# Optimization experiments

Hardware: AMD Instinct MI355X
Metric: run time of the kernel (lower is better)

## Reference

```python
import jax, jax.numpy as jnp
import numpy as np

N = 50000
E = 800000
IN_FEATS = 256
NUM_HEADS = 4
OUT_FEATS = 64
NUM_ETYPES = 8
ALPHA = 100.0
NEG_SLOPE_ATTN = 0.2   # self.leaky_relu
NEG_SLOPE_EW = 0.01    # nn.LeakyReLU() default, applied to edge weights


def leaky_relu(x, slope):
    return jnp.where(x >= 0, x, slope * x)


def setup_inputs() -> dict:
    key = jax.random.key(0)
    ks = jax.random.split(key, 8)
    feat = jax.random.normal(ks[0], (N, IN_FEATS), dtype=jnp.float32)
    src = jax.random.randint(ks[1], (E,), 0, N, dtype=jnp.int32)
    dst = jax.random.randint(ks[2], (E,), 0, N, dtype=jnp.int32)
    # etypes are 1-indexed in the original code (edge_weight[edge_feats - 1])
    edge_feats = jax.random.randint(ks[3], (E,), 1, NUM_ETYPES + 1, dtype=jnp.int32)
    # parameters (xavier-normal-ish init for weights; edge_weight = 1/alpha)
    fc_w = jax.random.normal(ks[4], (NUM_HEADS * OUT_FEATS, IN_FEATS), dtype=jnp.float32) * 0.05
    attn_l = jax.random.normal(ks[5], (1, NUM_HEADS, OUT_FEATS), dtype=jnp.float32) * 0.1
    attn_r = jax.random.normal(ks[6], (1, NUM_HEADS, OUT_FEATS), dtype=jnp.float32) * 0.1
    edge_weight = jnp.full((NUM_ETYPES, NUM_HEADS), 1.0 / ALPHA, dtype=jnp.float32)
    return {"feat": feat, "src": src, "dst": dst, "edge_feats": edge_feats,
            "fc_w": fc_w, "attn_l": attn_l, "attn_r": attn_r, "edge_weight": edge_weight}


def reference(feat, src, dst, edge_feats, fc_w, attn_l, attn_r, edge_weight):
    # feat: [N, F_in] -> ft: [N, H, D]
    ft = (feat @ fc_w.T).reshape(-1, NUM_HEADS, OUT_FEATS)
    el = jnp.einsum('nhd,ohd->nh', ft, attn_l)  # [N, H]
    er = jnp.einsum('nhd,ohd->nh', ft, attn_r)  # [N, H]
    # edge-type weights (1-indexed), scaled & leaky-relu'd
    ew = leaky_relu(edge_weight * ALPHA, NEG_SLOPE_EW)  # [T, H]
    ee = ew[edge_feats - 1]                              # [E, H]
    # per-edge logits: u_add_v, times edge weight, leaky relu
    e = leaky_relu((el[src] + er[dst]) * ee, NEG_SLOPE_ATTN)  # [E, H]
    # edge softmax grouped by destination node
    emax = jax.ops.segment_max(e, dst, num_segments=N)        # [N, H]
    ex = jnp.exp(e - emax[dst])
    denom = jax.ops.segment_sum(ex, dst, num_segments=N)      # [N, H]
    a = ex / denom[dst]                                        # [E, H]
    # weighted scatter-sum: sum over edges of a * ft[src]
    msg = ft[src] * a[:, :, None]                              # [E, H, D]
    rst = jax.ops.segment_sum(msg, dst, num_segments=N)       # [N, H, D]
    return rst
```

## Files before the change

### kernel.cpp

```cpp
#include <hip/hip_runtime.h>
#include <hip/hip_bf16.h>


#define NF 256
#define HD 256
#define NH 4
#define PB 256

typedef __attribute__((ext_vector_type(8))) short short8;
typedef __attribute__((ext_vector_type(4))) float f32x4;

static __device__ __forceinline__ unsigned short f2bf(float f) {
  unsigned int u = __float_as_uint(f);
  u += 0x7FFFu + ((u >> 16) & 1u);
  return (unsigned short)(u >> 16);
}
static __device__ __forceinline__ float bf2f(unsigned short s) {
  return __uint_as_float(((unsigned int)s) << 16);
}
static __device__ __forceinline__ unsigned pkbf(float a, float b) {
  __hip_bfloat162 h = __float22bfloat162_rn(make_float2(a, b));
  return *(unsigned*)&h;
}
static __device__ __forceinline__ float wcalc(float sum, float ew) {
  float x = sum * ew;
  x = (x >= 0.f) ? x : 0.2f * x;
  return __expf(x);
}

__global__ __launch_bounds__(256) void part_hist_k(
    const int* __restrict__ dst, const float* __restrict__ w,
    unsigned short* __restrict__ o, int* __restrict__ ghist, int e, int epb) {
  __shared__ int bins[256];
  int tid = threadIdx.x, blk = blockIdx.x;
  bins[tid] = 0;
  int ci = blk * 256 + tid;
  if (ci < 16384) {
    float4 v = ((const float4*)w)[ci];
    ((uint2*)o)[ci] = make_uint2(pkbf(v.x, v.y), pkbf(v.z, v.w));
  }
  __syncthreads();
  int e0 = blk * epb, e1 = e0 + epb; if (e1 > e) e1 = e;
  for (int i = e0 + tid; i < e1; i += 256)
    atomicAdd(&bins[dst[i] >> 8], 1);
  __syncthreads();
  ghist[tid * PB + blk] = bins[tid];
}

__global__ __launch_bounds__(1024) void scan2_k(const int* __restrict__ in,
                                                int* __restrict__ outp, int n) {
  __shared__ int wtot[16];
  __shared__ int wexcl[16];
  __shared__ int ctot;
  int tid = threadIdx.x, lane = tid & 63, wid = tid >> 6;
  int carry = 0;
  int nchunk = (n + 8191) >> 13;
  for (int c = 0; c < nchunk; ++c) {
    int base = (c << 13) + tid * 8;
    int v[8];
    if (base + 8 <= n) {
      int4 a = *(const int4*)(in + base);
      int4 b = *(const int4*)(in + base + 4);
      v[0] = a.x; v[1] = a.y; v[2] = a.z; v[3] = a.w;
      v[4] = b.x; v[5] = b.y; v[6] = b.z; v[7] = b.w;
    } else {
#pragma unroll
      for (int j = 0; j < 8; ++j) v[j] = (base + j < n) ? in[base + j] : 0;
    }
    int p[8]; int run = 0;
#pragma unroll
    for (int j = 0; j < 8; ++j) { run += v[j]; p[j] = run; }
    int incl = run;
#pragma unroll
    for (int off = 1; off < 64; off <<= 1) {
      int t = __shfl_up(incl, off);
      if (lane >= off) incl += t;
    }
    if (lane == 63) wtot[wid] = incl;
    __syncthreads();
    if (wid == 0 && lane < 16) {
      int wv = wtot[lane]; int wi = wv;
#pragma unroll
      for (int off = 1; off < 16; off <<= 1) {
        int t = __shfl_up(wi, off);
        if (lane >= off) wi += t;
      }
      wexcl[lane] = wi - wv;
      if (lane == 15) ctot = wi;
    }
    __syncthreads();
    int ebase = carry + wexcl[wid] + (incl - run);
#pragma unroll
    for (int j = 0; j < 8; ++j) {
      int i = base + j;
      if (i < n) outp[i] = ebase + p[j] - v[j];
    }
    carry += ctot;
    __syncthreads();
  }
  if (tid == 0) outp[n] = carry;
}

__global__ __launch_bounds__(256) void part_scatter_k(
    const int* __restrict__ src, const int* __restrict__ dst,
    const int* __restrict__ efeats, const int* __restrict__ sg,
    int* __restrict__ mid, int e, int epb) {
  __shared__ int cur[256];
  int tid = threadIdx.x, blk = blockIdx.x;
  cur[tid] = sg[tid * PB + blk];
  __syncthreads();
  int e0 = blk * epb, e1 = e0 + epb; if (e1 > e) e1 = e;
  for (int i = e0 + tid; i < e1; i += 256) {
    int d = dst[i];
    int pos = atomicAdd(&cur[d >> 8], 1);
    mid[pos] = src[i] | ((efeats[i] - 1) << 17) | ((d & 255) << 20);
  }
}

__global__ __launch_bounds__(256) void bucket_k(
    const int* __restrict__ mid, const int* __restrict__ sg,
    int* __restrict__ poffs, int* __restrict__ pk, int nN) {
  __shared__ int cnt[256];
  __shared__ int cur[256];
  int tid = threadIdx.x, b = blockIdx.x;
  int bb0 = sg[b * PB];
  int bb1 = sg[(b + 1) * PB];
  cnt[tid] = 0;
  __syncthreads();
  for (int i = bb0 + tid; i < bb1; i += 256)
    atomicAdd(&cnt[(mid[i] >> 20) & 255], 1);
  __syncthreads();
  if (tid < 64) {
    int carry = 0;
#pragma unroll
    for (int c = 0; c < 4; ++c) {
      int v = cnt[c * 64 + tid];
      int inc = v;
#pragma unroll
      for (int off = 1; off < 64; off <<= 1) {
        int t2 = __shfl_up(inc, off);
        if (tid >= off) inc += t2;
      }
      cur[c * 64 + tid] = inc - v + carry;
      carry += __shfl(inc, 63);
    }
  }
  __syncthreads();
  int node = b * 256 + tid;
  int g = bb0 + cur[tid];
  if (node <= nN) poffs[node] = g;
  cur[tid] = g;
  __syncthreads();
  for (int i = bb0 + tid; i < bb1; i += 256) {
    int v = mid[i];
    int pos = atomicAdd(&cur[(v >> 20) & 255], 1);
    pk[pos] = v & 0xFFFFF;
  }
}

__global__ __launch_bounds__(256) void gemm_k(
    const float* __restrict__ feat, const unsigned short* __restrict__ fcb,
    const float* __restrict__ attn_l, const float* __restrict__ attn_r,
    unsigned short* __restrict__ ftb, float* __restrict__ el,
    float* __restrict__ er, int n) {
  __shared__ short aF[4 * 2 * 64 * 8];
  __shared__ short bF[16 * 2 * 64 * 8];
  int tid = threadIdx.x;
  int lane = tid & 63, w = tid >> 6;
  int row0 = blockIdx.x * 64;

  f32x4 acc[4][4];
#pragma unroll
  for (int i = 0; i < 4; ++i)
#pragma unroll
    for (int j = 0; j < 4; ++j) acc[i][j] = (f32x4){0.f, 0.f, 0.f, 0.f};

  int ar = tid >> 2, ak = (tid & 3) << 4;
  int arow = row0 + ar; if (arow >= n) arow = n - 1;
  const float* ap = feat + (size_t)arow * NF + ak;
  int am = ar & 15, art = ar >> 4;
  int s0 = ak >> 5, q0 = (ak >> 3) & 3;
  int s1 = (ak + 8) >> 5, q1 = ((ak + 8) >> 3) & 3;
  short* aw0 = &aF[(((art * 2 + s0) * 64) + q0 * 16 + am) * 8];
  short* aw1 = &aF[(((art * 2 + s1) * 64) + q1 * 16 + am) * 8];

  const unsigned short* bp = fcb + (size_t)tid * NF;
  int bn = tid & 15, bcg = tid >> 4;

  for (int k0 = 0; k0 < NF; k0 += 64) {
    float4 f0 = *(const float4*)(ap + k0);
    float4 f1 = *(const float4*)(ap + k0 + 4);
    float4 f2 = *(const float4*)(ap + k0 + 8);
    float4 f3 = *(const float4*)(ap + k0 + 12);
    uint4 oa = make_uint4(pkbf(f0.x, f0.y), pkbf(f0.z, f0.w),
                          pkbf(f1.x, f1.y), pkbf(f1.z, f1.w));
    uint4 ob = make_uint4(pkbf(f2.x, f2.y), pkbf(f2.z, f2.w),
                          pkbf(f3.x, f3.y), pkbf(f3.z, f3.w));
    *(uint4*)aw0 = oa;
    *(uint4*)aw1 = ob;
#pragma unroll
    for (int o8 = 0; o8 < 8; ++o8) {
      short8 bv = *(const short8*)(bp + k0 + o8 * 8);
      int bs = o8 >> 2, bq = o8 & 3;
      *(short8*)&bF[(((bcg * 2 + bs) * 64) + bq * 16 + bn) * 8] = bv;
    }
    __syncthreads();
#pragma unroll
    for (int s = 0; s < 2; ++s) {
      short8 af[4], bfr[4];
#pragma unroll
      for (int rt = 0; rt < 4; ++rt)
        af[rt] = *(const short8*)&aF[(((rt * 2 + s) * 64) + lane) * 8];
#pragma unroll
      for (int ct = 0; ct < 4; ++ct)
        bfr[ct] = *(const short8*)&bF[((((w * 4 + ct) * 2 + s) * 64) + lane) * 8];
#pragma unroll
      for (int rt = 0; rt < 4; ++rt)
#pragma unroll
        for (int ct = 0; ct < 4; ++ct)
          acc[rt][ct] = __builtin_amdgcn_mfma_f32_16x16x32_bf16(
              af[rt], bfr[ct], acc[rt][ct], 0, 0, 0);
    }
    __syncthreads();
  }

  int ln = lane & 15, lq = lane >> 4;
  float al4[4], ar4[4];
#pragma unroll
  for (int ct = 0; ct < 4; ++ct) {
    al4[ct] = attn_l[w * 64 + ct * 16 + ln];
    ar4[ct] = attn_r[w * 64 + ct * 16 + ln];
  }
#pragma unroll
  for (int rt = 0; rt < 4; ++rt) {
#pragma unroll
    for (int r = 0; r < 4; ++r) {
      float pl = 0.f, pr = 0.f;
#pragma unroll
      for (int ct = 0; ct < 4; ++ct) {
        float v = acc[rt][ct][r];
        pl += v * al4[ct]; pr += v * ar4[ct];
      }
#pragma unroll
      for (int off = 1; off <= 8; off <<= 1) {
        pl += __shfl_xor(pl, off);
        pr += __shfl_xor(pr, off);
      }
      int row = row0 + rt * 16 + lq * 4 + r;
      if (row < n) {
        if (ln == 0) { el[row * NH + w] = pl; er[row * NH + w] = pr; }
        unsigned short* fr = ftb + (size_t)row * HD + w * 64 + ln;
#pragma unroll
        for (int ct = 0; ct < 4; ++ct) fr[ct * 16] = f2bf(acc[rt][ct][r]);
      }
    }
  }
}

__global__ __launch_bounds__(256) void agg3_k(
    const unsigned short* __restrict__ ftb, const int* __restrict__ pk,
    const float* __restrict__ el, const float* __restrict__ er,
    const float* __restrict__ ewt, const int* __restrict__ offs,
    float* __restrict__ out, int n) {
  __shared__ float ew_s[32];
  if (threadIdx.x < 32) {
    float v = ewt[threadIdx.x] * 100.0f;
    ew_s[threadIdx.x] = (v >= 0.f) ? v : 0.01f * v;
  }
  __syncthreads();
  int node = blockIdx.x * 4 + (threadIdx.x >> 6);
  int lane = threadIdx.x & 63;
  if (node >= n) return;
  int start = offs[node];
  int deg = offs[node + 1] - start;
  float o0 = 0.f, o1 = 0.f, o2 = 0.f, o3 = 0.f;
  if (deg > 0) {
    int hl = lane >> 4;
    float er_h = er[(size_t)node * NH + hl];
    const unsigned short* fb = ftb + (size_t)lane * 4;
    const float* elh = el + hl;
    const int* pg = pk + start;
    float ss = 0.f;
    int i = 0;
    for (; i + 8 <= deg; i += 8) {
      int4 pa = *(const int4*)(pg + i);
      int4 pb = *(const int4*)(pg + i + 4);
      int sA = pa.x & 0x1FFFF, tA = pa.x >> 17;
      int sB = pa.y & 0x1FFFF, tB = pa.y >> 17;
      int sC = pa.z & 0x1FFFF, tC = pa.z >> 17;
      int sD = pa.w & 0x1FFFF, tD = pa.w >> 17;
      int sE = pb.x & 0x1FFFF, tE = pb.x >> 17;
      int sF = pb.y & 0x1FFFF, tF = pb.y >> 17;
      int sG = pb.z & 0x1FFFF, tG = pb.z >> 17;
      int sH = pb.w & 0x1FFFF, tH = pb.w >> 17;
      float eA = elh[sA * NH], eB = elh[sB * NH], eC = elh[sC * NH], eD = elh[sD * NH];
      float eE = elh[sE * NH], eF = elh[sF * NH], eG = elh[sG * NH], eH = elh[sH * NH];
      ushort4 fA = *(const ushort4*)(fb + (size_t)sA * HD);
      ushort4 fB = *(const ushort4*)(fb + (size_t)sB * HD);
      ushort4 fC = *(const ushort4*)(fb + (size_t)sC * HD);
      ushort4 fD = *(const ushort4*)(fb + (size_t)sD * HD);
      ushort4 fE = *(const ushort4*)(fb + (size_t)sE * HD);
      ushort4 fF = *(const ushort4*)(fb + (size_t)sF * HD);
      ushort4 fG = *(const ushort4*)(fb + (size_t)sG * HD);
      ushort4 fH = *(const ushort4*)(fb + (size_t)sH * HD);
      float wA = wcalc(eA + er_h, ew_s[tA * NH + hl]);
      float wB = wcalc(eB + er_h, ew_s[tB * NH + hl]);
      float wC = wcalc(eC + er_h, ew_s[tC * NH + hl]);
      float wD = wcalc(eD + er_h, ew_s[tD * NH + hl]);
      float wE = wcalc(eE + er_h, ew_s[tE * NH + hl]);
      float wF = wcalc(eF + er_h, ew_s[tF * NH + hl]);
      float wG = wcalc(eG + er_h, ew_s[tG * NH + hl]);
      float wH = wcalc(eH + er_h, ew_s[tH * NH + hl]);
      ss += ((wA + wB) + (wC + wD)) + ((wE + wF) + (wG + wH));
      o0 = fmaf(wA, bf2f(fA.x), o0); o1 = fmaf(wA, bf2f(fA.y), o1);
      o2 = fmaf(wA, bf2f(fA.z), o2); o3 = fmaf(wA, bf2f(fA.w), o3);
      o0 = fmaf(wB, bf2f(fB.x), o0); o1 = fmaf(wB, bf2f(fB.y), o1);
      o2 = fmaf(wB, bf2f(fB.z), o2); o3 = fmaf(wB, bf2f(fB.w), o3);
      o0 = fmaf(wC, bf2f(fC.x), o0); o1 = fmaf(wC, bf2f(fC.y), o1);
      o2 = fmaf(wC, bf2f(fC.z), o2); o3 = fmaf(wC, bf2f(fC.w), o3);
      o0 = fmaf(wD, bf2f(fD.x), o0); o1 = fmaf(wD, bf2f(fD.y), o1);
      o2 = fmaf(wD, bf2f(fD.z), o2); o3 = fmaf(wD, bf2f(fD.w), o3);
      o0 = fmaf(wE, bf2f(fE.x), o0); o1 = fmaf(wE, bf2f(fE.y), o1);
      o2 = fmaf(wE, bf2f(fE.z), o2); o3 = fmaf(wE, bf2f(fE.w), o3);
      o0 = fmaf(wF, bf2f(fF.x), o0); o1 = fmaf(wF, bf2f(fF.y), o1);
      o2 = fmaf(wF, bf2f(fF.z), o2); o3 = fmaf(wF, bf2f(fF.w), o3);
      o0 = fmaf(wG, bf2f(fG.x), o0); o1 = fmaf(wG, bf2f(fG.y), o1);
      o2 = fmaf(wG, bf2f(fG.z), o2); o3 = fmaf(wG, bf2f(fG.w), o3);
      o0 = fmaf(wH, bf2f(fH.x), o0); o1 = fmaf(wH, bf2f(fH.y), o1);
      o2 = fmaf(wH, bf2f(fH.z), o2); o3 = fmaf(wH, bf2f(fH.w), o3);
    }
    for (; i < deg; ++i) {
      int pv = pg[i];
      int sA = pv & 0x1FFFF, tA = pv >> 17;
      float eA = elh[sA * NH];
      ushort4 fA = *(const ushort4*)(fb + (size_t)sA * HD);
      float wA = wcalc(eA + er_h, ew_s[tA * NH + hl]);
      ss += wA;
      o0 = fmaf(wA, bf2f(fA.x), o0); o1 = fmaf(wA, bf2f(fA.y), o1);
      o2 = fmaf(wA, bf2f(fA.z), o2); o3 = fmaf(wA, bf2f(fA.w), o3);
    }
    float rs = 1.0f / ss;
    o0 *= rs; o1 *= rs; o2 *= rs; o3 *= rs;
  }
  *(float4*)(out + (size_t)node * HD + lane * 4) = make_float4(o0, o1, o2, o3);
}

extern "C" void kernel_launch(void* const* d_in, const int* in_sizes, int n_in,
                              void* d_out, int out_size, void* d_ws, size_t ws_size,
                              hipStream_t stream) {
  const float* feat   = (const float*)d_in[0];
  const int*   src    = (const int*)d_in[1];
  const int*   dst    = (const int*)d_in[2];
  const int*   efeats = (const int*)d_in[3];
  const float* fc_w   = (const float*)d_in[4];
  const float* attn_l = (const float*)d_in[5];
  const float* attn_r = (const float*)d_in[6];
  const float* ewt    = (const float*)d_in[7];
  float* out = (float*)d_out;

  int N = in_sizes[0] / NF;
  int E = in_sizes[1];

  char* ws = (char*)d_ws;
  size_t off = 0;
  unsigned short* fcb = (unsigned short*)(ws + off); off += (size_t)NF * HD * 2;
  unsigned short* ftb = (unsigned short*)(ws + off); off += (size_t)N * HD * 2;
  float* el  = (float*)(ws + off);  off += (size_t)N * NH * 4;
  float* er  = (float*)(ws + off);  off += (size_t)N * NH * 4;
  int* poffs = (int*)(ws + off);    off += ((size_t)N + 16) * 4;
  int* ghist = (int*)(ws + off);    off += (size_t)PB * 256 * 4;
  int* sg    = (int*)(ws + off);    off += ((size_t)PB * 256 + 8) * 4;
  int* mid   = (int*)(ws + off);    off += (size_t)E * 4;
  int* pk    = (int*)(ws + off);    off += (size_t)E * 4;

  int epb = (E + PB - 1) / PB;
  int NB = (N >> 8) + 1;

  part_hist_k<<<PB, 256, 0, stream>>>(dst, fc_w, fcb, ghist, E, epb);
  scan2_k<<<1, 1024, 0, stream>>>(ghist, sg, PB * 256);
  part_scatter_k<<<PB, 256, 0, stream>>>(src, dst, efeats, sg, mid, E, epb);
  bucket_k<<<NB, 256, 0, stream>>>(mid, sg, poffs, pk, N);
  gemm_k<<<(N + 63) / 64, 256, 0, stream>>>(feat, fcb, attn_l, attn_r, ftb, el, er, N);
  agg3_k<<<(N + 3) / 4, 256, 0, stream>>>(ftb, pk, el, er, ewt, poffs, out, N);
}
```

Baseline: 270.7 us.

## Fuse all stages into one persistent cooperative kernel with grid syncs

Merges the six separate launches (histogram, scan, partition scatter, bucket sort, GEMM, aggregation) into one cooperative persistent kernel. Stages are separated by grid-wide barriers, and work is spread with grid-stride loops. The single-block global scan becomes a two-level multi-block scan. This aims to remove per-launch gaps and the serial scan bottleneck. In exchange it pays for grid-barrier latency, an occupancy query on every call, and a register cap from the launch bounds that may slow the GEMM and aggregation phases. The old multi-kernel path is kept as a fallback.

```diff
diff --git a/kernel.cpp b/kernel.cpp
--- a/kernel.cpp
+++ b/kernel.cpp
@@ -1,11 +1,13 @@
 #include <hip/hip_runtime.h>
 #include <hip/hip_bf16.h>
+#include <hip/hip_cooperative_groups.h>
+
+namespace cg = cooperative_groups;
 
 
 #define NF 256
 #define HD 256
 #define NH 4
-#define PB 256
 
 typedef __attribute__((ext_vector_type(8))) short short8;
 typedef __attribute__((ext_vector_type(4))) float f32x4;
@@ -28,147 +30,12 @@
   return __expf(x);
 }
 
-__global__ __launch_bounds__(256) void part_hist_k(
-    const int* __restrict__ dst, const float* __restrict__ w,
-    unsigned short* __restrict__ o, int* __restrict__ ghist, int e, int epb) {
-  __shared__ int bins[256];
-  int tid = threadIdx.x, blk = blockIdx.x;
-  bins[tid] = 0;
-  int ci = blk * 256 + tid;
-  if (ci < 16384) {
-    float4 v = ((const float4*)w)[ci];
-    ((uint2*)o)[ci] = make_uint2(pkbf(v.x, v.y), pkbf(v.z, v.w));
-  }
-  __syncthreads();
-  int e0 = blk * epb, e1 = e0 + epb; if (e1 > e) e1 = e;
-  for (int i = e0 + tid; i < e1; i += 256)
-    atomicAdd(&bins[dst[i] >> 8], 1);
-  __syncthreads();
-  ghist[tid * PB + blk] = bins[tid];
-}
-
-__global__ __launch_bounds__(1024) void scan2_k(const int* __restrict__ in,
-                                                int* __restrict__ outp, int n) {
-  __shared__ int wtot[16];
-  __shared__ int wexcl[16];
-  __shared__ int ctot;
-  int tid = threadIdx.x, lane = tid & 63, wid = tid >> 6;
-  int carry = 0;
-  int nchunk = (n + 8191) >> 13;
-  for (int c = 0; c < nchunk; ++c) {
-    int base = (c << 13) + tid * 8;
-    int v[8];
-    if (base + 8 <= n) {
-      int4 a = *(const int4*)(in + base);
-      int4 b = *(const int4*)(in + base + 4);
-      v[0] = a.x; v[1] = a.y; v[2] = a.z; v[3] = a.w;
-      v[4] = b.x; v[5] = b.y; v[6] = b.z; v[7] = b.w;
-    } else {
-#pragma unroll
-      for (int j = 0; j < 8; ++j) v[j] = (base + j < n) ? in[base + j] : 0;
-    }
-    int p[8]; int run = 0;
-#pragma unroll
-    for (int j = 0; j < 8; ++j) { run += v[j]; p[j] = run; }
-    int incl = run;
-#pragma unroll
-    for (int off = 1; off < 64; off <<= 1) {
-      int t = __shfl_up(incl, off);
-      if (lane >= off) incl += t;
-    }
-    if (lane == 63) wtot[wid] = incl;
-    __syncthreads();
-    if (wid == 0 && lane < 16) {
-      int wv = wtot[lane]; int wi = wv;
-#pragma unroll
-      for (int off = 1; off < 16; off <<= 1) {
-        int t = __shfl_up(wi, off);
-        if (lane >= off) wi += t;
-      }
-      wexcl[lane] = wi - wv;
-      if (lane == 15) ctot = wi;
-    }
-    __syncthreads();
-    int ebase = carry + wexcl[wid] + (incl - run);
-#pragma unroll
-    for (int j = 0; j < 8; ++j) {
-      int i = base + j;
-      if (i < n) outp[i] = ebase + p[j] - v[j];
-    }
-    carry += ctot;
-    __syncthreads();
-  }
-  if (tid == 0) outp[n] = carry;
-}
-
-__global__ __launch_bounds__(256) void part_scatter_k(
-    const int* __restrict__ src, const int* __restrict__ dst,
-    const int* __restrict__ efeats, const int* __restrict__ sg,
-    int* __restrict__ mid, int e, int epb) {
-  __shared__ int cur[256];
-  int tid = threadIdx.x, blk = blockIdx.x;
-  cur[tid] = sg[tid * PB + blk];
-  __syncthreads();
-  int e0 = blk * epb, e1 = e0 + epb; if (e1 > e) e1 = e;
-  for (int i = e0 + tid; i < e1; i += 256) {
-    int d = dst[i];
-    int pos = atomicAdd(&cur[d >> 8], 1);
-    mid[pos] = src[i] | ((efeats[i] - 1) << 17) | ((d & 255) << 20);
-  }
-}
-
-__global__ __launch_bounds__(256) void bucket_k(
-    const int* __restrict__ mid, const int* __restrict__ sg,
-    int* __restrict__ poffs, int* __restrict__ pk, int nN) {
-  __shared__ int cnt[256];
-  __shared__ int cur[256];
-  int tid = threadIdx.x, b = blockIdx.x;
-  int bb0 = sg[b * PB];
-  int bb1 = sg[(b + 1) * PB];
-  cnt[tid] = 0;
-  __syncthreads();
-  for (int i = bb0 + tid; i < bb1; i += 256)
-    atomicAdd(&cnt[(mid[i] >> 20) & 255], 1);
-  __syncthreads();
-  if (tid < 64) {
-    int carry = 0;
-#pragma unroll
-    for (int c = 0; c < 4; ++c) {
-      int v = cnt[c * 64 + tid];
-      int inc = v;
-#pragma unroll
-      for (int off = 1; off < 64; off <<= 1) {
-        int t2 = __shfl_up(inc, off);
-        if (tid >= off) inc += t2;
-      }
-      cur[c * 64 + tid] = inc - v + carry;
-      carry += __shfl(inc, 63);
-    }
-  }
-  __syncthreads();
-  int node = b * 256 + tid;
-  int g = bb0 + cur[tid];
-  if (node <= nN) poffs[node] = g;
-  cur[tid] = g;
-  __syncthreads();
-  for (int i = bb0 + tid; i < bb1; i += 256) {
-    int v = mid[i];
-    int pos = atomicAdd(&cur[(v >> 20) & 255], 1);
-    pk[pos] = v & 0xFFFFF;
-  }
-}
-
-__global__ __launch_bounds__(256) void gemm_k(
-    const float* __restrict__ feat, const unsigned short* __restrict__ fcb,
-    const float* __restrict__ attn_l, const float* __restrict__ attn_r,
-    unsigned short* __restrict__ ftb, float* __restrict__ el,
-    float* __restrict__ er, int n) {
-  __shared__ short aF[4 * 2 * 64 * 8];
-  __shared__ short bF[16 * 2 * 64 * 8];
-  int tid = threadIdx.x;
+
+static __device__ __forceinline__ void gemm_tile(
+    const float* feat, const unsigned short* fcb, const float* attn_l,
+    const float* attn_r, unsigned short* ftb, float* el, float* er,
+    int n, int row0, int tid, short* aF, short* bF) {
   int lane = tid & 63, w = tid >> 6;
-  int row0 = blockIdx.x * 64;
-
   f32x4 acc[4][4];
 #pragma unroll
   for (int i = 0; i < 4; ++i)
@@ -257,22 +124,11 @@
   }
 }
 
-__global__ __launch_bounds__(256) void agg3_k(
-    const unsigned short* __restrict__ ftb, const int* __restrict__ pk,
-    const float* __restrict__ el, const float* __restrict__ er,
-    const float* __restrict__ ewt, const int* __restrict__ offs,
-    float* __restrict__ out, int n) {
-  __shared__ float ew_s[32];
-  if (threadIdx.x < 32) {
-    float v = ewt[threadIdx.x] * 100.0f;
-    ew_s[threadIdx.x] = (v >= 0.f) ? v : 0.01f * v;
-  }
-  __syncthreads();
-  int node = blockIdx.x * 4 + (threadIdx.x >> 6);
-  int lane = threadIdx.x & 63;
-  if (node >= n) return;
-  int start = offs[node];
-  int deg = offs[node + 1] - start;
+static __device__ __forceinline__ void agg_node(
+    const unsigned short* ftb, const int* pk, const float* el, const float* er,
+    const float* ew_s, const int* poffs, float* out, int node, int lane) {
+  int start = poffs[node];
+  int deg = poffs[node + 1] - start;
   float o0 = 0.f, o1 = 0.f, o2 = 0.f, o3 = 0.f;
   if (deg > 0) {
     int hl = lane >> 4;
@@ -345,6 +201,327 @@
   *(float4*)(out + (size_t)node * HD + lane * 4) = make_float4(o0, o1, o2, o3);
 }
 
+
+__global__ __launch_bounds__(256, 4) void mega_k(
+    const float* __restrict__ feat, const float* __restrict__ fc_w,
+    const int* __restrict__ src, const int* __restrict__ dst,
+    const int* __restrict__ efeats, const float* __restrict__ attn_l,
+    const float* __restrict__ attn_r, const float* __restrict__ ewt,
+    unsigned short* fcb, unsigned short* ftb, float* el, float* er,
+    int* ghist, int* sg, int* btot, int* bbase, int* mid, int* pk,
+    int* poffs, float* out, int n, int e) {
+  cg::grid_group gg = cg::this_grid();
+  __shared__ __align__(16) char smem[40960];
+  int tid = threadIdx.x, blk = blockIdx.x;
+  int nblk = gridDim.x;
+  int lane = tid & 63, wid = tid >> 6;
+  int epb = (e + nblk - 1) / nblk;
+  int e0 = blk * epb, e1 = e0 + epb; if (e1 > e) e1 = e;
+
+  {
+    int* bins = (int*)smem;
+    bins[tid] = 0;
+    int ci = blk * 256 + tid;
+    if (ci < 16384) {
+      float4 v = ((const float4*)fc_w)[ci];
+      ((uint2*)fcb)[ci] = make_uint2(pkbf(v.x, v.y), pkbf(v.z, v.w));
+    }
+    __syncthreads();
+    for (int i = e0 + tid; i < e1; i += 256)
+      atomicAdd(&bins[dst[i] >> 8], 1);
+    __syncthreads();
+    ghist[tid * nblk + blk] = bins[tid];
+  }
+  gg.sync();
+
+  {
+    int* wt = (int*)smem;
+    int v = ghist[blk * 256 + tid];
+    int inc = v;
+#pragma unroll
+    for (int off = 1; off < 64; off <<= 1) {
+      int t = __shfl_up(inc, off);
+      if (lane >= off) inc += t;
+    }
+    if (lane == 63) wt[wid] = inc;
+    __syncthreads();
+    int base = 0;
+    if (wid > 0) base += wt[0];
+    if (wid > 1) base += wt[1];
+    if (wid > 2) base += wt[2];
+    sg[blk * 256 + tid] = base + inc - v;
+    if (tid == 255) btot[blk] = base + inc;
+  }
+  gg.sync();
+
+  if (blk == 0) {
+    int* wt = (int*)smem;
+    int per = nblk >> 8;
+    int vals[4]; int run = 0;
+#pragma unroll
+    for (int k = 0; k < 4; ++k) {
+      vals[k] = (k < per) ? btot[tid * per + k] : 0;
+      run += vals[k];
+    }
+    int inc = run;
+#pragma unroll
+    for (int off = 1; off < 64; off <<= 1) {
+      int t = __shfl_up(inc, off);
+      if (lane >= off) inc += t;
+    }
+    if (lane == 63) wt[wid] = inc;
+    __syncthreads();
+    int base = 0;
+    if (wid > 0) base += wt[0];
+    if (wid > 1) base += wt[1];
+    if (wid > 2) base += wt[2];
+    int eb = base + inc - run;
+#pragma unroll
+    for (int k = 0; k < 4; ++k)
+      if (k < per) { bbase[tid * per + k] = eb; eb += vals[k]; }
+  }
+  gg.sync();
+
+  {
+    int* cur = (int*)smem;
+    int j = tid * nblk + blk;
+    cur[tid] = sg[j] + bbase[j >> 8];
+    __syncthreads();
+    for (int i = e0 + tid; i < e1; i += 256) {
+      int d = dst[i];
+      int pos = atomicAdd(&cur[d >> 8], 1);
+      mid[pos] = src[i] | ((efeats[i] - 1) << 17) | ((d & 255) << 20);
+    }
+  }
+  gg.sync();
+
+  {
+    int nbuck = (n + 255) >> 8;
+    int* cnt = (int*)smem;
+    int* cur = (int*)smem + 256;
+    for (int b = blk; b < nbuck; b += nblk) {
+      int j0 = b * nblk, j1 = (b + 1) * nblk;
+      int bb0 = sg[j0] + bbase[j0 >> 8];
+      int bb1 = sg[j1] + bbase[j1 >> 8];
+      cnt[tid] = 0;
+      __syncthreads();
+      for (int i = bb0 + tid; i < bb1; i += 256)
+        atomicAdd(&cnt[(mid[i] >> 20) & 255], 1);
+      __syncthreads();
+      if (tid < 64) {
+        int carry = 0;
+#pragma unroll
+        for (int c = 0; c < 4; ++c) {
+          int v = cnt[c * 64 + tid];
+          int inc = v;
+#pragma unroll
+          for (int off = 1; off < 64; off <<= 1) {
+            int t2 = __shfl_up(inc, off);
+            if (tid >= off) inc += t2;
+          }
+          cur[c * 64 + tid] = inc - v + carry;
+          carry += __shfl(inc, 63);
+        }
+      }
+      __syncthreads();
+      int node = b * 256 + tid;
+      int gv = bb0 + cur[tid];
+      if (node <= n) poffs[node] = gv;
+      cur[tid] = gv;
+      __syncthreads();
+      for (int i = bb0 + tid; i < bb1; i += 256) {
+        int v = mid[i];
+        int pos = atomicAdd(&cur[(v >> 20) & 255], 1);
+        pk[pos] = v & 0xFFFFF;
+      }
+      __syncthreads();
+    }
+  }
+  __syncthreads();
+
+  {
+    short* aF = (short*)smem;
+    short* bF = (short*)(smem + 8192);
+    for (int t = blk; t * 64 < n; t += nblk)
+      gemm_tile(feat, fcb, attn_l, attn_r, ftb, el, er, n, t * 64, tid, aF, bF);
+  }
+  gg.sync();
+
+  {
+    float* ew_s = (float*)smem;
+    if (tid < 32) {
+      float v = ewt[tid] * 100.0f;
+      ew_s[tid] = (v >= 0.f) ? v : 0.01f * v;
+    }
+    __syncthreads();
+    for (int nb = blk * 4; nb < n; nb += nblk * 4) {
+      int node = nb + wid;
+      if (node < n) agg_node(ftb, pk, el, er, ew_s, poffs, out, node, lane);
+    }
+  }
+}
+
+
+__global__ __launch_bounds__(256) void part_hist_k(
+    const int* __restrict__ dst, const float* __restrict__ w,
+    unsigned short* __restrict__ o, int* __restrict__ ghist, int e, int epb,
+    int pb) {
+  __shared__ int bins[256];
+  int tid = threadIdx.x, blk = blockIdx.x;
+  bins[tid] = 0;
+  int ci = blk * 256 + tid;
+  if (ci < 16384) {
+    float4 v = ((const float4*)w)[ci];
+    ((uint2*)o)[ci] = make_uint2(pkbf(v.x, v.y), pkbf(v.z, v.w));
+  }
+  __syncthreads();
+  int e0 = blk * epb, e1 = e0 + epb; if (e1 > e) e1 = e;
+  for (int i = e0 + tid; i < e1; i += 256)
+    atomicAdd(&bins[dst[i] >> 8], 1);
+  __syncthreads();
+  ghist[tid * pb + blk] = bins[tid];
+}
+
+__global__ __launch_bounds__(1024) void scan2_k(const int* __restrict__ in,
+                                                int* __restrict__ outp, int n) {
+  __shared__ int wtot[16];
+  __shared__ int wexcl[16];
+  __shared__ int ctot;
+  int tid = threadIdx.x, lane = tid & 63, wid = tid >> 6;
+  int carry = 0;
+  int nchunk = (n + 8191) >> 13;
+  for (int c = 0; c < nchunk; ++c) {
+    int base = (c << 13) + tid * 8;
+    int v[8];
+    if (base + 8 <= n) {
+      int4 a = *(const int4*)(in + base);
+      int4 b = *(const int4*)(in + base + 4);
+      v[0] = a.x; v[1] = a.y; v[2] = a.z; v[3] = a.w;
+      v[4] = b.x; v[5] = b.y; v[6] = b.z; v[7] = b.w;
+    } else {
+#pragma unroll
+      for (int j = 0; j < 8; ++j) v[j] = (base + j < n) ? in[base + j] : 0;
+    }
+    int p[8]; int run = 0;
+#pragma unroll
+    for (int j = 0; j < 8; ++j) { run += v[j]; p[j] = run; }
+    int incl = run;
+#pragma unroll
+    for (int off = 1; off < 64; off <<= 1) {
+      int t = __shfl_up(incl, off);
+      if (lane >= off) incl += t;
+    }
+    if (lane == 63) wtot[wid] = incl;
+    __syncthreads();
+    if (wid == 0 && lane < 16) {
+      int wv = wtot[lane]; int wi = wv;
+#pragma unroll
+      for (int off = 1; off < 16; off <<= 1) {
+        int t = __shfl_up(wi, off);
+        if (lane >= off) wi += t;
+      }
+      wexcl[lane] = wi - wv;
+      if (lane == 15) ctot = wi;
+    }
+    __syncthreads();
+    int ebase = carry + wexcl[wid] + (incl - run);
+#pragma unroll
+    for (int j = 0; j < 8; ++j) {
+      int i = base + j;
+      if (i < n) outp[i] = ebase + p[j] - v[j];
+    }
+    carry += ctot;
+    __syncthreads();
+  }
+  if (tid == 0) outp[n] = carry;
+}
+
+__global__ __launch_bounds__(256) void part_scatter_k(
+    const int* __restrict__ src, const int* __restrict__ dst,
+    const int* __restrict__ efeats, const int* __restrict__ sg,
+    int* __restrict__ mid, int e, int epb, int pb) {
+  __shared__ int cur[256];
+  int tid = threadIdx.x, blk = blockIdx.x;
+  cur[tid] = sg[tid * pb + blk];
+  __syncthreads();
+  int e0 = blk * epb, e1 = e0 + epb; if (e1 > e) e1 = e;
+  for (int i = e0 + tid; i < e1; i += 256) {
+    int d = dst[i];
+    int pos = atomicAdd(&cur[d >> 8], 1);
+    mid[pos] = src[i] | ((efeats[i] - 1) << 17) | ((d & 255) << 20);
+  }
+}
+
+__global__ __launch_bounds__(256) void bucket_k(
+    const int* __restrict__ mid, const int* __restrict__ sg,
+    int* __restrict__ poffs, int* __restrict__ pk, int nN, int pb) {
+  __shared__ int cnt[256];
+  __shared__ int cur[256];
+  int tid = threadIdx.x, b = blockIdx.x;
+  int bb0 = sg[b * pb];
+  int bb1 = sg[(b + 1) * pb];
+  cnt[tid] = 0;
+  __syncthreads();
+  for (int i = bb0 + tid; i < bb1; i += 256)
+    atomicAdd(&cnt[(mid[i] >> 20) & 255], 1);
+  __syncthreads();
+  if (tid < 64) {
+    int carry = 0;
+#pragma unroll
+    for (int c = 0; c < 4; ++c) {
+      int v = cnt[c * 64 + tid];
+      int inc = v;
+#pragma unroll
+      for (int off = 1; off < 64; off <<= 1) {
+        int t2 = __shfl_up(inc, off);
+        if (tid >= off) inc += t2;
+      }
+      cur[c * 64 + tid] = inc - v + carry;
+      carry += __shfl(inc, 63);
+    }
+  }
+  __syncthreads();
+  int node = b * 256 + tid;
+  int g = bb0 + cur[tid];
+  if (node <= nN) poffs[node] = g;
+  cur[tid] = g;
+  __syncthreads();
+  for (int i = bb0 + tid; i < bb1; i += 256) {
+    int v = mid[i];
+    int pos = atomicAdd(&cur[(v >> 20) & 255], 1);
+    pk[pos] = v & 0xFFFFF;
+  }
+}
+
+__global__ __launch_bounds__(256) void gemm_k(
+    const float* __restrict__ feat, const unsigned short* __restrict__ fcb,
+    const float* __restrict__ attn_l, const float* __restrict__ attn_r,
+    unsigned short* __restrict__ ftb, float* __restrict__ el,
+    float* __restrict__ er, int n) {
+  __shared__ short aF[4 * 2 * 64 * 8];
+  __shared__ short bF[16 * 2 * 64 * 8];
+  gemm_tile(feat, fcb, attn_l, attn_r, ftb, el, er, n,
+            blockIdx.x * 64, threadIdx.x, aF, bF);
+}
+
+__global__ __launch_bounds__(256) void agg3_k(
+    const unsigned short* __restrict__ ftb, const int* __restrict__ pk,
+    const float* __restrict__ el, const float* __restrict__ er,
+    const float* __restrict__ ewt, const int* __restrict__ offs,
+    float* __restrict__ out, int n) {
+  __shared__ float ew_s[32];
+  if (threadIdx.x < 32) {
+    float v = ewt[threadIdx.x] * 100.0f;
+    ew_s[threadIdx.x] = (v >= 0.f) ? v : 0.01f * v;
+  }
+  __syncthreads();
+  int node = blockIdx.x * 4 + (threadIdx.x >> 6);
+  int lane = threadIdx.x & 63;
+  if (node >= n) return;
+  agg_node(ftb, pk, el, er, ew_s, offs, out, node, lane);
+}
+
+
 extern "C" void kernel_launch(void* const* d_in, const int* in_sizes, int n_in,
                               void* d_out, int out_size, void* d_ws, size_t ws_size,
                               hipStream_t stream) {
@@ -368,18 +545,36 @@
   float* el  = (float*)(ws + off);  off += (size_t)N * NH * 4;
   float* er  = (float*)(ws + off);  off += (size_t)N * NH * 4;
   int* poffs = (int*)(ws + off);    off += ((size_t)N + 16) * 4;
-  int* ghist = (int*)(ws + off);    off += (size_t)PB * 256 * 4;
-  int* sg    = (int*)(ws + off);    off += ((size_t)PB * 256 + 8) * 4;
+  int* ghist = (int*)(ws + off);    off += (size_t)1024 * 256 * 4;
+  int* sg    = (int*)(ws + off);    off += ((size_t)1024 * 256 + 8) * 4;
+  int* btot  = (int*)(ws + off);    off += 1024 * 4;
+  int* bbase = (int*)(ws + off);    off += 1024 * 4;
   int* mid   = (int*)(ws + off);    off += (size_t)E * 4;
   int* pk    = (int*)(ws + off);    off += (size_t)E * 4;
 
-  int epb = (E + PB - 1) / PB;
-  int NB = (N >> 8) + 1;
-
-  part_hist_k<<<PB, 256, 0, stream>>>(dst, fc_w, fcb, ghist, E, epb);
-  scan2_k<<<1, 1024, 0, stream>>>(ghist, sg, PB * 256);
-  part_scatter_k<<<PB, 256, 0, stream>>>(src, dst, efeats, sg, mid, E, epb);
-  bucket_k<<<NB, 256, 0, stream>>>(mid, sg, poffs, pk, N);
-  gemm_k<<<(N + 63) / 64, 256, 0, stream>>>(feat, fcb, attn_l, attn_r, ftb, el, er, N);
-  agg3_k<<<(N + 3) / 4, 256, 0, stream>>>(ftb, pk, el, er, ewt, poffs, out, N);
-}
+  int occ = 0;
+  hipError_t oerr = hipOccupancyMaxActiveBlocksPerMultiprocessor(&occ, mega_k, 256, 0);
+  bool coop_ok = (oerr == hipSuccess) && (occ >= 1);
+  if (coop_ok) {
+    if (occ > 4) occ = 4;
+    int nblk = occ * 256;
+    void* args[] = {&feat, &fc_w, &src, &dst, &efeats, &attn_l, &attn_r, &ewt,
+                    &fcb, &ftb, &el, &er, &ghist, &sg, &btot, &bbase,
+                    &mid, &pk, &poffs, &out, &N, &E};
+    hipError_t lerr = hipLaunchCooperativeKernel(mega_k, dim3(nblk), dim3(256),
+                                                 args, 0, stream);
+    if (lerr != hipSuccess) { (void)hipGetLastError(); coop_ok = false; }
+  }
+
+  if (!coop_ok) {
+    int pb = 256;
+    int epb = (E + pb - 1) / pb;
+    int nbuck = (N + 255) >> 8;
+    part_hist_k<<<pb, 256, 0, stream>>>(dst, fc_w, fcb, ghist, E, epb, pb);
+    scan2_k<<<1, 1024, 0, stream>>>(ghist, sg, pb * 256);
+    part_scatter_k<<<pb, 256, 0, stream>>>(src, dst, efeats, sg, mid, E, epb, pb);
+    bucket_k<<<nbuck, 256, 0, stream>>>(mid, sg, poffs, pk, N, pb);
+    gemm_k<<<(N + 63) / 64, 256, 0, stream>>>(feat, fcb, attn_l, attn_r, ftb, el, er, N);
+    agg3_k<<<(N + 3) / 4, 256, 0, stream>>>(ftb, pk, el, er, ewt, poffs, out, N);
+  }
+}
```

After: 603.1 us. 2.23x slower.

## Fuse edge partition scatter into GEMM launch via block-index split

Applied to the files above, without the earlier changes.

The separate edge-scatter kernel is merged into the GEMM kernel. The first sb blocks perform the bucket scatter using the GEMM's shared memory as their counter array, and the remaining blocks run the node-feature GEMM, so the two independent stages overlap on the GPU. The partition block count becomes a runtime value, 1024 minus the number of GEMM blocks, and it is passed through to the histogram, scan and bucket kernels. Bucket sorting now runs after the fused launch. This removes one kernel launch and fills the GPU better, but it changes how edges are split into partitions, and the scatter blocks may compete with the GEMM blocks for memory bandwidth.

```diff
diff --git a/kernel.cpp b/kernel.cpp
--- a/kernel.cpp
+++ b/kernel.cpp
@@ -5,7 +5,6 @@
 #define NF 256
 #define HD 256
 #define NH 4
-#define PB 256
 
 typedef __attribute__((ext_vector_type(8))) short short8;
 typedef __attribute__((ext_vector_type(4))) float f32x4;
@@ -30,7 +29,8 @@
 
 __global__ __launch_bounds__(256) void part_hist_k(
     const int* __restrict__ dst, const float* __restrict__ w,
-    unsigned short* __restrict__ o, int* __restrict__ ghist, int e, int epb) {
+    unsigned short* __restrict__ o, int* __restrict__ ghist, int e, int epb,
+    int pb) {
   __shared__ int bins[256];
   int tid = threadIdx.x, blk = blockIdx.x;
   bins[tid] = 0;
@@ -44,7 +44,7 @@
   for (int i = e0 + tid; i < e1; i += 256)
     atomicAdd(&bins[dst[i] >> 8], 1);
   __syncthreads();
-  ghist[tid * PB + blk] = bins[tid];
+  ghist[tid * pb + blk] = bins[tid];
 }
 
 __global__ __launch_bounds__(1024) void scan2_k(const int* __restrict__ in,
@@ -101,73 +101,34 @@
   if (tid == 0) outp[n] = carry;
 }
 
-__global__ __launch_bounds__(256) void part_scatter_k(
-    const int* __restrict__ src, const int* __restrict__ dst,
-    const int* __restrict__ efeats, const int* __restrict__ sg,
-    int* __restrict__ mid, int e, int epb) {
-  __shared__ int cur[256];
-  int tid = threadIdx.x, blk = blockIdx.x;
-  cur[tid] = sg[tid * PB + blk];
-  __syncthreads();
-  int e0 = blk * epb, e1 = e0 + epb; if (e1 > e) e1 = e;
-  for (int i = e0 + tid; i < e1; i += 256) {
-    int d = dst[i];
-    int pos = atomicAdd(&cur[d >> 8], 1);
-    mid[pos] = src[i] | ((efeats[i] - 1) << 17) | ((d & 255) << 20);
-  }
-}
-
-__global__ __launch_bounds__(256) void bucket_k(
-    const int* __restrict__ mid, const int* __restrict__ sg,
-    int* __restrict__ poffs, int* __restrict__ pk, int nN) {
-  __shared__ int cnt[256];
-  __shared__ int cur[256];
-  int tid = threadIdx.x, b = blockIdx.x;
-  int bb0 = sg[b * PB];
-  int bb1 = sg[(b + 1) * PB];
-  cnt[tid] = 0;
-  __syncthreads();
-  for (int i = bb0 + tid; i < bb1; i += 256)
-    atomicAdd(&cnt[(mid[i] >> 20) & 255], 1);
-  __syncthreads();
-  if (tid < 64) {
-    int carry = 0;
-#pragma unroll
-    for (int c = 0; c < 4; ++c) {
-      int v = cnt[c * 64 + tid];
-      int inc = v;
-#pragma unroll
-      for (int off = 1; off < 64; off <<= 1) {
-        int t2 = __shfl_up(inc, off);
-        if (tid >= off) inc += t2;
-      }
-      cur[c * 64 + tid] = inc - v + carry;
-      carry += __shfl(inc, 63);
-    }
-  }
-  __syncthreads();
-  int node = b * 256 + tid;
-  int g = bb0 + cur[tid];
-  if (node <= nN) poffs[node] = g;
-  cur[tid] = g;
-  __syncthreads();
-  for (int i = bb0 + tid; i < bb1; i += 256) {
-    int v = mid[i];
-    int pos = atomicAdd(&cur[(v >> 20) & 255], 1);
-    pk[pos] = v & 0xFFFFF;
-  }
-}
-
-__global__ __launch_bounds__(256) void gemm_k(
+__global__ __launch_bounds__(256) void fused_k(
     const float* __restrict__ feat, const unsigned short* __restrict__ fcb,
     const float* __restrict__ attn_l, const float* __restrict__ attn_r,
     unsigned short* __restrict__ ftb, float* __restrict__ el,
-    float* __restrict__ er, int n) {
+    float* __restrict__ er, int n,
+    const int* __restrict__ src, const int* __restrict__ dst,
+    const int* __restrict__ efeats, const int* __restrict__ sg,
+    int* __restrict__ mid, int e, int epb, int sb) {
   __shared__ short aF[4 * 2 * 64 * 8];
   __shared__ short bF[16 * 2 * 64 * 8];
   int tid = threadIdx.x;
+
+  if (blockIdx.x < sb) {
+    int* cur = (int*)aF;
+    int blk = blockIdx.x;
+    cur[tid] = sg[tid * sb + blk];
+    __syncthreads();
+    int e0 = blk * epb, e1 = e0 + epb; if (e1 > e) e1 = e;
+    for (int i = e0 + tid; i < e1; i += 256) {
+      int d = dst[i];
+      int pos = atomicAdd(&cur[d >> 8], 1);
+      mid[pos] = src[i] | ((efeats[i] - 1) << 17) | ((d & 255) << 20);
+    }
+    return;
+  }
+
   int lane = tid & 63, w = tid >> 6;
-  int row0 = blockIdx.x * 64;
+  int row0 = (blockIdx.x - sb) * 64;
 
   f32x4 acc[4][4];
 #pragma unroll
@@ -254,6 +215,47 @@
         for (int ct = 0; ct < 4; ++ct) fr[ct * 16] = f2bf(acc[rt][ct][r]);
       }
     }
+  }
+}
+
+__global__ __launch_bounds__(256) void bucket_k(
+    const int* __restrict__ mid, const int* __restrict__ sg,
+    int* __restrict__ poffs, int* __restrict__ pk, int nN, int pb) {
+  __shared__ int cnt[256];
+  __shared__ int cur[256];
+  int tid = threadIdx.x, b = blockIdx.x;
+  int bb0 = sg[b * pb];
+  int bb1 = sg[(b + 1) * pb];
+  cnt[tid] = 0;
+  __syncthreads();
+  for (int i = bb0 + tid; i < bb1; i += 256)
+    atomicAdd(&cnt[(mid[i] >> 20) & 255], 1);
+  __syncthreads();
+  if (tid < 64) {
+    int carry = 0;
+#pragma unroll
+    for (int c = 0; c < 4; ++c) {
+      int v = cnt[c * 64 + tid];
+      int inc = v;
+#pragma unroll
+      for (int off = 1; off < 64; off <<= 1) {
+        int t2 = __shfl_up(inc, off);
+        if (tid >= off) inc += t2;
+      }
+      cur[c * 64 + tid] = inc - v + carry;
+      carry += __shfl(inc, 63);
+    }
+  }
+  __syncthreads();
+  int node = b * 256 + tid;
+  int g = bb0 + cur[tid];
+  if (node <= nN) poffs[node] = g;
+  cur[tid] = g;
+  __syncthreads();
+  for (int i = bb0 + tid; i < bb1; i += 256) {
+    int v = mid[i];
+    int pos = atomicAdd(&cur[(v >> 20) & 255], 1);
+    pk[pos] = v & 0xFFFFF;
   }
 }
 
@@ -368,18 +370,20 @@
   float* el  = (float*)(ws + off);  off += (size_t)N * NH * 4;
   float* er  = (float*)(ws + off);  off += (size_t)N * NH * 4;
   int* poffs = (int*)(ws + off);    off += ((size_t)N + 16) * 4;
-  int* ghist = (int*)(ws + off);    off += (size_t)PB * 256 * 4;
-  int* sg    = (int*)(ws + off);    off += ((size_t)PB * 256 + 8) * 4;
+  int* ghist = (int*)(ws + off);    off += (size_t)256 * 256 * 4;
+  int* sg    = (int*)(ws + off);    off += ((size_t)256 * 256 + 8) * 4;
   int* mid   = (int*)(ws + off);    off += (size_t)E * 4;
   int* pk    = (int*)(ws + off);    off += (size_t)E * 4;
 
-  int epb = (E + PB - 1) / PB;
-  int NB = (N >> 8) + 1;
-
-  part_hist_k<<<PB, 256, 0, stream>>>(dst, fc_w, fcb, ghist, E, epb);
-  scan2_k<<<1, 1024, 0, stream>>>(ghist, sg, PB * 256);
-  part_scatter_k<<<PB, 256, 0, stream>>>(src, dst, efeats, sg, mid, E, epb);
-  bucket_k<<<NB, 256, 0, stream>>>(mid, sg, poffs, pk, N);
-  gemm_k<<<(N + 63) / 64, 256, 0, stream>>>(feat, fcb, attn_l, attn_r, ftb, el, er, N);
+  int gb = (N + 63) / 64;
+  int sb = 1024 - gb;
+  int epb = (E + sb - 1) / sb;
+  int nbuck = (N + 255) >> 8;
+
+  part_hist_k<<<sb, 256, 0, stream>>>(dst, fc_w, fcb, ghist, E, epb, sb);
+  scan2_k<<<1, 1024, 0, stream>>>(ghist, sg, 256 * sb);
+  fused_k<<<sb + gb, 256, 0, stream>>>(feat, fcb, attn_l, attn_r, ftb, el, er, N,
+                                       src, dst, efeats, sg, mid, E, epb, sb);
+  bucket_k<<<nbuck, 256, 0, stream>>>(mid, sg, poffs, pk, N, sb);
   agg3_k<<<(N + 3) / 4, 256, 0, stream>>>(ftb, pk, el, er, ewt, poffs, out, N);
 }
```

Result: faster. 259.9 us (-4.0%).
